# Performance work log

Hardware: AMD Instinct MI355X
Metric: run time of the kernel (lower is better)

## Reference

```python
import jax, jax.numpy as jnp
import numpy as np

EMB = 64
NODE_DIM = 5
T = 5
B, N = 8, 512


def setup_inputs() -> dict:
    key = jax.random.key(0)
    ks = jax.random.split(key, 24)
    def w(k, shape):
        return jax.random.normal(k, shape, dtype=jnp.float32) * 0.1
    xv = jax.random.normal(ks[0], (B, N, NODE_DIM), dtype=jnp.float32)
    Ws = jax.random.uniform(ks[1], (B, N, N), dtype=jnp.float32)
    reach = jax.random.bernoulli(ks[2], 0.5, (B, N))
    reach = reach.at[:, 0].set(True)  # guarantee at least one reachable node
    return {
        'xv': xv, 'Ws': Ws, 'reachable_nodes': reach,
        'W1a': w(ks[3], (NODE_DIM, EMB)), 'b1a': w(ks[4], (EMB,)),
        'W1b': w(ks[5], (EMB, EMB)),      'b1b': w(ks[6], (EMB,)),
        'W2':  w(ks[7], (EMB, EMB)),      'b2':  w(ks[8], (EMB,)),
        'W3':  w(ks[9], (EMB, EMB)),      'b3':  w(ks[10], (EMB,)),
        'w4':  w(ks[11], (EMB,)),         'b4':  w(ks[12], (EMB,)),
        'W6':  w(ks[13], (EMB, EMB)),     'b6':  w(ks[14], (EMB,)),
        'W7':  w(ks[15], (EMB, EMB)),     'b7':  w(ks[16], (EMB,)),
        'W51': w(ks[17], (2 * EMB, EMB)), 'b51': w(ks[18], (EMB,)),
        'w52': w(ks[19], (EMB,)),         'b52': w(ks[20], ()),
    }


def _struc2vec(xv, Ws, W1a, b1a, W1b, b1b, W2, b2, W3, b3, w4, b4):
    # s1: per-node feature embedding [B,N,E]
    s1 = jax.nn.relu(xv @ W1a + b1a) @ W1b + b1b
    # edge-feature path: relu(theta4(Ws[...,None])) summed over dim 1 -> [B,N,E]
    s3_1 = jax.nn.relu(Ws[..., None] * w4 + b4)  # [B,N,N,E]
    s3 = jnp.sum(s3_1, axis=1) @ W3 + b3         # [B,N,E]
    mu = jnp.zeros(s1.shape, dtype=s1.dtype)
    for _ in range(T):
        s2 = jnp.einsum('bnm,bme->bne', Ws, mu) @ W2 + b2
        mu = jax.nn.relu(s1 + s2 + s3)
    return mu


def reference(xv, Ws, reachable_nodes, W1a, b1a, W1b, b1b, W2, b2, W3, b3,
              w4, b4, W6, b6, W7, b7, W51, b51, w52, b52):
    mu = _struc2vec(xv, Ws, W1a, b1a, W1b, b1b, W2, b2, W3, b3, w4, b4)
    # global state broadcast to every node + local per-node action embedding
    global_state = jnp.sum(mu, axis=1, keepdims=True) @ W6 + b6  # [B,1,E]
    global_state = jnp.broadcast_to(global_state, mu.shape)      # [B,N,E]
    local_action = mu @ W7 + b7                                  # [B,N,E]
    rep = jax.nn.relu(jnp.concatenate([global_state, local_action], axis=2))
    rep = jax.nn.relu(rep) @ W51 + b51                           # relu(relu(.)) as in source
    prob_logits = rep @ w52 + b52                                # [B,N]
    prob_logits = jnp.where(reachable_nodes, prob_logits, -jnp.inf)
    return prob_logits
```

## Files before the change

### kernel.cpp

```cpp
#include <hip/hip_runtime.h>
#include <hip/hip_bf16.h>
#include <cstdint>
#include <cstddef>

#define BB 8
#define NN 512
#define EE 64

typedef __attribute__((ext_vector_type(8))) short short8v;
typedef __attribute__((ext_vector_type(4))) float f32x4;
typedef __attribute__((ext_vector_type(4))) unsigned int u32x4;
typedef __attribute__((ext_vector_type(2))) unsigned int u32x2;

static __device__ __forceinline__ unsigned short f2bf(float f) {
  __hip_bfloat16 h = __float2bfloat16(f);
  return *reinterpret_cast<unsigned short*>(&h);
}
static __device__ __forceinline__ float bf2f(unsigned short u) {
  unsigned x = ((unsigned)u) << 16;
  float f; __builtin_memcpy(&f, &x, 4); return f;
}
static __device__ __forceinline__ u32x4 ld_b128_sc(const void* p) {
  u32x4 v;
  asm volatile("global_load_dwordx4 %0, %1, off sc0 sc1"
               : "=v"(v) : "v"(p) : "memory");
  return v;
}
static __device__ __forceinline__ unsigned ld_b32_sc(const void* p) {
  unsigned v;
  asm volatile("global_load_dword %0, %1, off sc0 sc1\n\ts_waitcnt vmcnt(0)"
               : "=v"(v) : "v"(p) : "memory");
  return v;
}
static __device__ __forceinline__ void st_b64_sc(void* p, u32x2 v) {
  asm volatile("global_store_dwordx2 %0, %1, off sc0 sc1"
               :: "v"(p), "v"(v) : "memory");
}
static __device__ __forceinline__ void st_b32_sc(void* p, unsigned v) {
  asm volatile("global_store_dword %0, %1, off sc0 sc1"
               :: "v"(p), "v"(v) : "memory");
}
static __device__ __forceinline__ void vm0() {
  asm volatile("s_waitcnt vmcnt(0)" ::: "memory");
}
static __device__ __forceinline__ short8v as_s8(u32x4 v) {
  short8v r; __builtin_memcpy(&r, &v, 16); return r;
}

__global__ __launch_bounds__(512) void k_fused(
    const float* __restrict__ Ws, const float* __restrict__ xv,
    const float* __restrict__ W1a, const float* __restrict__ b1a,
    const float* __restrict__ W1b, const float* __restrict__ b1b,
    const float* __restrict__ W2, const float* __restrict__ b2,
    const float* __restrict__ W3, const float* __restrict__ b3,
    const float* __restrict__ w4, const float* __restrict__ b4,
    const float* __restrict__ W6, const float* __restrict__ b6,
    const float* __restrict__ W7, const float* __restrict__ b7,
    const float* __restrict__ W51, const float* __restrict__ b51,
    const float* __restrict__ w52, const float* __restrict__ b52,
    const void* __restrict__ reach, float* __restrict__ out,
    unsigned short* __restrict__ zA, unsigned short* __restrict__ zB,
    float* __restrict__ gpart, unsigned* __restrict__ flags) {
  const int blk = blockIdx.x;
  const int b = blk >> 5;
  const int stripe = blk & 31;
  const int n0 = stripe << 4;
  const int t = threadIdx.x;
  const int w = t >> 6, l = t & 63, lr = l & 15, hi = l >> 4;
  const int lk = hi * 8, nq = hi * 4, eb = w & 3, kh = w >> 2;

  __shared__ __attribute__((aligned(16))) float tileT[16][132];
  __shared__ float sp[16][68];
  __shared__ float half_[16][68];
  __shared__ float hh[16][68];
  __shared__ float base_lds[16][68];
  __shared__ float yred[16][68];
  __shared__ __attribute__((aligned(16))) unsigned short muzA[512];
  __shared__ __attribute__((aligned(16))) unsigned short muzB[512];
  __shared__ __attribute__((aligned(16))) unsigned short zbf[64][20];
  __shared__ float gsl[64], gsr[64], v7l[64], w52l[64], pl_lds[16];
  __shared__ float g0c;
  __shared__ int sbig, sflt;

  auto arrive = [&](int idx) {
    vm0();
    __syncthreads();
    if (t == 0) st_b32_sc(&flags[(b * 8 + idx) * 32 + stripe], 1u);
  };
  auto wait = [&](int idx) {
    if (t < 64) {
      const unsigned* fp = &flags[(b * 8 + idx) * 32 + (t & 31)];
      while (true) {
        unsigned v = ld_b32_sc(fp);
        if (__ballot(v != 0u) == ~0ull) break;
        __builtin_amdgcn_s_sleep(1);
      }
    }
    __syncthreads();
  };

  auto muz_store = [&](int node, int e, float v) {
    int eh = e & 31;
    unsigned short* dst = (e < 32) ? muzA : muzB;
    dst[((eh >> 3) * 16 + node) * 8 + (eh & 7)] = f2bf(v);
  };

  const float* wsbase = Ws + (size_t)b * NN * NN;
  const int lrow = t >> 2, lc4 = (t & 3) * 4;
  float4 tr0 = *(const float4*)&wsbase[(size_t)(0 * 128 + lrow) * NN + n0 + lc4];
  float4 tr1 = *(const float4*)&wsbase[(size_t)(1 * 128 + lrow) * NN + n0 + lc4];
  float4 tr2 = *(const float4*)&wsbase[(size_t)(2 * 128 + lrow) * NN + n0 + lc4];
  float4 tr3 = *(const float4*)&wsbase[(size_t)(3 * 128 + lrow) * NN + n0 + lc4];

  short8v WBa = {}, WBb = {};
  if (w < 4) {
    union { unsigned short u[8]; short8v v; } pa, pb;
#pragma unroll
    for (int j = 0; j < 8; ++j) {
      pa.u[j] = f2bf(W2[(8 * hi + j) * EE + 16 * w + lr]);
      pb.u[j] = f2bf(W2[(8 * hi + j + 32) * EE + 16 * w + lr]);
    }
    WBa = pa.v; WBb = pb.v;
  }

  {
    int e = t & 63;
#pragma unroll
    for (int p = 0; p < 2; ++p) {
      int rr = p * 8 + (t >> 6);
      const float* x = xv + ((size_t)b * NN + n0 + rr) * 5;
      float h = b1a[e];
      h = fmaf(x[0], W1a[0 * EE + e], h);
      h = fmaf(x[1], W1a[1 * EE + e], h);
      h = fmaf(x[2], W1a[2 * EE + e], h);
      h = fmaf(x[3], W1a[3 * EE + e], h);
      h = fmaf(x[4], W1a[4 * EE + e], h);
      hh[rr][e] = fmaxf(h, 0.f);
    }
  }
  {
    int ih = t >> 8;
    int n = (t >> 4) & 15;
    int e0 = (t & 15) * 4;
    float4 w4v = *(const float4*)&w4[e0];
    float4 b4v = *(const float4*)&b4[e0];
    float a0 = 0.f, a1 = 0.f, a2 = 0.f, a3 = 0.f;
    int ib = ih * 64;
#pragma unroll
    for (int c = 0; c < 4; ++c) {
      float4 tv = (c == 0) ? tr0 : (c == 1) ? tr1 : (c == 2) ? tr2 : tr3;
      tileT[lc4 + 0][lrow] = tv.x;
      tileT[lc4 + 1][lrow] = tv.y;
      tileT[lc4 + 2][lrow] = tv.z;
      tileT[lc4 + 3][lrow] = tv.w;
      __syncthreads();
#pragma unroll
      for (int i4 = 0; i4 < 16; ++i4) {
        float4 wv = *(const float4*)&tileT[n][ib + i4 * 4];
#pragma unroll
        for (int k = 0; k < 4; ++k) {
          float ww = (k == 0) ? wv.x : (k == 1) ? wv.y : (k == 2) ? wv.z : wv.w;
          a0 += fmaxf(fmaf(ww, w4v.x, b4v.x), 0.f);
          a1 += fmaxf(fmaf(ww, w4v.y, b4v.y), 0.f);
          a2 += fmaxf(fmaf(ww, w4v.z, b4v.z), 0.f);
          a3 += fmaxf(fmaf(ww, w4v.w, b4v.w), 0.f);
        }
      }
      __syncthreads();
    }
    if (ih) {
      half_[n][e0] = a0; half_[n][e0 + 1] = a1;
      half_[n][e0 + 2] = a2; half_[n][e0 + 3] = a3;
    }
    __syncthreads();
    if (!ih) {
      sp[n][e0]     = a0 + half_[n][e0];
      sp[n][e0 + 1] = a1 + half_[n][e0 + 1];
      sp[n][e0 + 2] = a2 + half_[n][e0 + 2];
      sp[n][e0 + 3] = a3 + half_[n][e0 + 3];
    }
  }
  __syncthreads();
  {
    int e = t & 63;
#pragma unroll
    for (int p = 0; p < 2; ++p) {
      int rr = p * 8 + (t >> 6);
      float s = b1b[e] + b3[e] + b2[e];
#pragma unroll 8
      for (int j = 0; j < EE; ++j)
        s = fmaf(hh[rr][j], W1b[j * EE + e], fmaf(sp[rr][j], W3[j * EE + e], s));
      base_lds[rr][e] = s;
      muz_store(rr, e, fmaxf(s, 0.f));
    }
  }
  __syncthreads();

  auto zphase = [&]() {
    if (w < 4) {
      short8v a0 = *(const short8v*)&muzA[l * 8];
      short8v a1 = *(const short8v*)&muzB[l * 8];
      f32x4 zacc = {0.f, 0.f, 0.f, 0.f};
      zacc = __builtin_amdgcn_mfma_f32_16x16x32_bf16(a0, WBa, zacc, 0, 0, 0);
      zacc = __builtin_amdgcn_mfma_f32_16x16x32_bf16(a1, WBb, zacc, 0, 0, 0);
      ushort4 u;
      u.x = f2bf(zacc[0]); u.y = f2bf(zacc[1]);
      u.z = f2bf(zacc[2]); u.w = f2bf(zacc[3]);
      *(ushort4*)&zbf[16 * w + lr][4 * hi] = u;
    }
  };
  auto publish = [&](unsigned short* dst) {
    if (t < 256) {
      int e = t >> 2, mq = (t & 3) * 4;
      u32x2 v;
      __builtin_memcpy(&v, &zbf[e][mq], 8);
      st_b64_sc(dst + ((size_t)b * EE + e) * NN + n0 + mq, v);
    }
  };

  zphase();
  __syncthreads();
  publish(zA);
  arrive(0);

  short8v A0, A1, A2, A3, A4, A5, A6, A7;
  {
    const float* arow = wsbase + (size_t)(n0 + lr) * NN + kh * 256 + lk;
    union { unsigned short u[8]; short8v v; } pk;
#define LDA(DST, OFF)                                                        \
    { float4 fa = *(const float4*)(arow + OFF);                              \
      float4 fb = *(const float4*)(arow + OFF + 4);                          \
      pk.u[0] = f2bf(fa.x); pk.u[1] = f2bf(fa.y);                            \
      pk.u[2] = f2bf(fa.z); pk.u[3] = f2bf(fa.w);                            \
      pk.u[4] = f2bf(fb.x); pk.u[5] = f2bf(fb.y);                            \
      pk.u[6] = f2bf(fb.z); pk.u[7] = f2bf(fb.w);                            \
      DST = pk.v; }
    LDA(A0, 0)   LDA(A1, 32)  LDA(A2, 64)  LDA(A3, 96)
    LDA(A4, 128) LDA(A5, 160) LDA(A6, 192) LDA(A7, 224)
#undef LDA
  }

  auto prop = [&](const unsigned short* zsrc) {
    const unsigned short* Bp =
        zsrc + ((size_t)b * EE + eb * 16 + lr) * NN + kh * 256 + lk;
    u32x4 q0 = ld_b128_sc(Bp + 0);
    u32x4 q1 = ld_b128_sc(Bp + 32);
    u32x4 q2 = ld_b128_sc(Bp + 64);
    u32x4 q3 = ld_b128_sc(Bp + 96);
    u32x4 q4 = ld_b128_sc(Bp + 128);
    u32x4 q5 = ld_b128_sc(Bp + 160);
    u32x4 q6 = ld_b128_sc(Bp + 192);
    u32x4 q7 = ld_b128_sc(Bp + 224);
    vm0();
    __builtin_amdgcn_sched_barrier(0);
    f32x4 acc = {0.f, 0.f, 0.f, 0.f};
    acc = __builtin_amdgcn_mfma_f32_16x16x32_bf16(A0, as_s8(q0), acc, 0, 0, 0);
    acc = __builtin_amdgcn_mfma_f32_16x16x32_bf16(A1, as_s8(q1), acc, 0, 0, 0);
    acc = __builtin_amdgcn_mfma_f32_16x16x32_bf16(A2, as_s8(q2), acc, 0, 0, 0);
    acc = __builtin_amdgcn_mfma_f32_16x16x32_bf16(A3, as_s8(q3), acc, 0, 0, 0);
    acc = __builtin_amdgcn_mfma_f32_16x16x32_bf16(A4, as_s8(q4), acc, 0, 0, 0);
    acc = __builtin_amdgcn_mfma_f32_16x16x32_bf16(A5, as_s8(q5), acc, 0, 0, 0);
    acc = __builtin_amdgcn_mfma_f32_16x16x32_bf16(A6, as_s8(q6), acc, 0, 0, 0);
    acc = __builtin_amdgcn_mfma_f32_16x16x32_bf16(A7, as_s8(q7), acc, 0, 0, 0);
    if (kh == 1) {
#pragma unroll
      for (int q = 0; q < 4; ++q) yred[nq + q][eb * 16 + lr] = acc[q];
    }
    __syncthreads();
    if (kh == 0) {
      int ep = eb * 16 + lr;
#pragma unroll
      for (int q = 0; q < 4; ++q) {
        float v = fmaxf(base_lds[nq + q][ep] + acc[q] + yred[nq + q][ep], 0.f);
        muz_store(nq + q, ep, v);
      }
    }
    __syncthreads();
  };

  wait(0);
  prop(zA); zphase(); __syncthreads(); publish(zB); arrive(1); wait(1);
  prop(zB); zphase(); __syncthreads(); publish(zA); arrive(2); wait(2);
  prop(zA); zphase(); __syncthreads(); publish(zB); arrive(3); wait(3);
  prop(zB);

  if (t < 64) {
    int eh = t & 31, jj = t & 7, lb = (eh >> 3) * 16;
    const unsigned short* dst = (t < 32) ? muzA : muzB;
    float s = 0.f;
#pragma unroll
    for (int n = 0; n < 16; ++n) s += bf2f(dst[(lb + n) * 8 + jj]);
    st_b32_sc(&gpart[((size_t)b * 32 + stripe) * EE + t], __float_as_uint(s));
  }
  arrive(4);

  if (t == 0) { sbig = 0; sflt = 0; }
  if (t < 64) w52l[t] = w52[t];
  __syncthreads();
  if (t < 256) {
    const unsigned int* rw = (const unsigned int*)reach;
    bool big = false, flt = false;
#pragma unroll
    for (int l2 = 0; l2 < 4; ++l2) {
      unsigned int v = rw[t + l2 * 256];
      if (v > 1u) big = true;
      if (v == 0x3f800000u) flt = true;
    }
    if (big) sbig = 1;
    if (flt) sflt = 1;
  }
  if (t >= 320 && t < 384) {
    int j = t - 320;
    float v = 0.f;
#pragma unroll 8
    for (int e = 0; e < EE; ++e) v = fmaf(W51[(EE + j) * EE + e], w52[e], v);
    v7l[j] = v;
  }
  __syncthreads();
#pragma unroll
  for (int p = 0; p < 2; ++p) {
    int n = p * 8 + (t >> 6), e7 = t & 63;
    float la = b7[e7];
#pragma unroll
    for (int h = 0; h < 2; ++h) {
      const unsigned short* dst = h ? muzB : muzA;
#pragma unroll
      for (int h2 = 0; h2 < 4; ++h2) {
        short8v mv = *(const short8v*)&dst[(h2 * 16 + n) * 8];
#pragma unroll
        for (int j = 0; j < 8; ++j)
          la = fmaf(bf2f((unsigned short)mv[j]),
                    W7[(h * 32 + h2 * 8 + j) * EE + e7], la);
      }
    }
    float c = fmaxf(la, 0.f) * v7l[e7];
#pragma unroll
    for (int off = 32; off > 0; off >>= 1) c += __shfl_down(c, off, 64);
    if (e7 == 0) pl_lds[n] = c;
  }

  wait(4);

  float* gacc = &tileT[0][0];
  {
    int s = t >> 4, e4 = (t & 15) * 4;
    u32x4 v = ld_b128_sc(&gpart[((size_t)b * 32 + s) * EE + e4]);
    vm0();
    gacc[s * EE + e4 + 0] = __uint_as_float(v.x);
    gacc[s * EE + e4 + 1] = __uint_as_float(v.y);
    gacc[s * EE + e4 + 2] = __uint_as_float(v.z);
    gacc[s * EE + e4 + 3] = __uint_as_float(v.w);
  }
  __syncthreads();
  if (t < 64) {
    float s = 0.f;
#pragma unroll 8
    for (int k = 0; k < 32; ++k) s += gacc[k * EE + t];
    gsl[t] = s;
  }
  __syncthreads();
  if (t < 64) {
    float a = b6[t];
#pragma unroll 8
    for (int k = 0; k < EE; ++k) a = fmaf(gsl[k], W6[k * EE + t], a);
    gsr[t] = fmaxf(a, 0.f);
  }
  __syncthreads();
  if (t < 64) {
    float q = 0.f;
#pragma unroll 8
    for (int j = 0; j < EE; ++j) q = fmaf(gsr[j], W51[j * EE + t], q);
    float pg = (q + b51[t]) * w52l[t];
#pragma unroll
    for (int off = 32; off > 0; off >>= 1) pg += __shfl_down(pg, off, 64);
    if (t == 0) g0c = pg + b52[0];
  }
  __syncthreads();
  if (t < 16) {
    int row = b * NN + n0 + t;
    bool rc;
    if (sflt)      rc = ((const float*)reach)[row] != 0.f;
    else if (sbig) rc = ((const unsigned char*)reach)[row] != 0;
    else           rc = ((const int*)reach)[row] != 0;
    out[row] = rc ? (pl_lds[t] + g0c) : -1.0e30f;
  }
}

extern "C" void kernel_launch(void* const* d_in, const int* in_sizes, int n_in,
                              void* d_out, int out_size, void* d_ws, size_t ws_size,
                              hipStream_t stream) {
  const float* xv  = (const float*)d_in[0];
  const float* Ws  = (const float*)d_in[1];
  const void*  rch = d_in[2];
  const float* W1a = (const float*)d_in[3];
  const float* b1a = (const float*)d_in[4];
  const float* W1b = (const float*)d_in[5];
  const float* b1b = (const float*)d_in[6];
  const float* W2  = (const float*)d_in[7];
  const float* b2  = (const float*)d_in[8];
  const float* W3  = (const float*)d_in[9];
  const float* b3  = (const float*)d_in[10];
  const float* w4  = (const float*)d_in[11];
  const float* b4  = (const float*)d_in[12];
  const float* W6  = (const float*)d_in[13];
  const float* b6  = (const float*)d_in[14];
  const float* W7  = (const float*)d_in[15];
  const float* b7  = (const float*)d_in[16];
  const float* W51 = (const float*)d_in[17];
  const float* b51 = (const float*)d_in[18];
  const float* w52 = (const float*)d_in[19];
  const float* b52 = (const float*)d_in[20];
  float* out = (float*)d_out;

  char* wsb = (char*)d_ws;
  unsigned short* zA   = (unsigned short*)wsb;
  unsigned short* zB   = (unsigned short*)(wsb + (512 << 10));
  float* gpart         = (float*)(wsb + (1024 << 10));
  unsigned* flags      = (unsigned*)(wsb + (1088 << 10));

  hipMemsetAsync((void*)flags, 0, 8192, stream);
  k_fused<<<dim3(256), dim3(512), 0, stream>>>(
      Ws, xv, W1a, b1a, W1b, b1b, W2, b2, W3, b3, w4, b4,
      W6, b6, W7, b7, W51, b51, w52, b52, rch, out,
      zA, zB, gpart, flags);
}
```

Before: 56.55 us.

## Use four write-once z buffers, plain cached loads, and direct z stores

Replaces the two ping-pong z buffers with four separate workspace buffers, one per propagation round, so no global buffer is ever overwritten during the kernel. Because each buffer is written once, the propagation step can read it with ordinary vector loads instead of inline-asm sc0 sc1 loads with an explicit vmcnt wait and scheduling barrier. This lets the compiler interleave the loads with the MFMAs. The z-phase also stores its bf16 results straight to global memory from the MFMA lanes, removing the LDS staging tile, a block barrier and the separate publish pass. In exchange it doubles the workspace and relies on cross-XCD cache coherence holding for first-time reads of freshly written lines; the direct stores are also less regular than the staged ones.

```diff
diff --git a/kernel.cpp b/kernel.cpp
--- a/kernel.cpp
+++ b/kernel.cpp
@@ -42,9 +42,6 @@
 }
 static __device__ __forceinline__ void vm0() {
   asm volatile("s_waitcnt vmcnt(0)" ::: "memory");
-}
-static __device__ __forceinline__ short8v as_s8(u32x4 v) {
-  short8v r; __builtin_memcpy(&r, &v, 16); return r;
 }
 
 __global__ __launch_bounds__(512) void k_fused(
@@ -59,7 +56,8 @@
     const float* __restrict__ W51, const float* __restrict__ b51,
     const float* __restrict__ w52, const float* __restrict__ b52,
     const void* __restrict__ reach, float* __restrict__ out,
-    unsigned short* __restrict__ zA, unsigned short* __restrict__ zB,
+    unsigned short* __restrict__ z0, unsigned short* __restrict__ z1,
+    unsigned short* __restrict__ z2, unsigned short* __restrict__ z3,
     float* __restrict__ gpart, unsigned* __restrict__ flags) {
   const int blk = blockIdx.x;
   const int b = blk >> 5;
@@ -77,7 +75,6 @@
   __shared__ float yred[16][68];
   __shared__ __attribute__((aligned(16))) unsigned short muzA[512];
   __shared__ __attribute__((aligned(16))) unsigned short muzB[512];
-  __shared__ __attribute__((aligned(16))) unsigned short zbf[64][20];
   __shared__ float gsl[64], gsr[64], v7l[64], w52l[64], pl_lds[16];
   __shared__ float g0c;
   __shared__ int sbig, sflt;
@@ -196,7 +193,7 @@
   }
   __syncthreads();
 
-  auto zphase = [&]() {
+  auto zphase = [&](unsigned short* dst) {
     if (w < 4) {
       short8v a0 = *(const short8v*)&muzA[l * 8];
       short8v a1 = *(const short8v*)&muzB[l * 8];
@@ -206,21 +203,12 @@
       ushort4 u;
       u.x = f2bf(zacc[0]); u.y = f2bf(zacc[1]);
       u.z = f2bf(zacc[2]); u.w = f2bf(zacc[3]);
-      *(ushort4*)&zbf[16 * w + lr][4 * hi] = u;
+      u32x2 v; __builtin_memcpy(&v, &u, 8);
+      st_b64_sc(dst + ((size_t)b * EE + 16 * w + lr) * NN + n0 + 4 * hi, v);
     }
   };
-  auto publish = [&](unsigned short* dst) {
-    if (t < 256) {
-      int e = t >> 2, mq = (t & 3) * 4;
-      u32x2 v;
-      __builtin_memcpy(&v, &zbf[e][mq], 8);
-      st_b64_sc(dst + ((size_t)b * EE + e) * NN + n0 + mq, v);
-    }
-  };
-
-  zphase();
-  __syncthreads();
-  publish(zA);
+
+  zphase(z0);
   arrive(0);
 
   short8v A0, A1, A2, A3, A4, A5, A6, A7;
@@ -243,25 +231,23 @@
   auto prop = [&](const unsigned short* zsrc) {
     const unsigned short* Bp =
         zsrc + ((size_t)b * EE + eb * 16 + lr) * NN + kh * 256 + lk;
-    u32x4 q0 = ld_b128_sc(Bp + 0);
-    u32x4 q1 = ld_b128_sc(Bp + 32);
-    u32x4 q2 = ld_b128_sc(Bp + 64);
-    u32x4 q3 = ld_b128_sc(Bp + 96);
-    u32x4 q4 = ld_b128_sc(Bp + 128);
-    u32x4 q5 = ld_b128_sc(Bp + 160);
-    u32x4 q6 = ld_b128_sc(Bp + 192);
-    u32x4 q7 = ld_b128_sc(Bp + 224);
-    vm0();
-    __builtin_amdgcn_sched_barrier(0);
+    short8v q0 = *(const short8v*)(Bp + 0);
+    short8v q1 = *(const short8v*)(Bp + 32);
+    short8v q2 = *(const short8v*)(Bp + 64);
+    short8v q3 = *(const short8v*)(Bp + 96);
+    short8v q4 = *(const short8v*)(Bp + 128);
+    short8v q5 = *(const short8v*)(Bp + 160);
+    short8v q6 = *(const short8v*)(Bp + 192);
+    short8v q7 = *(const short8v*)(Bp + 224);
     f32x4 acc = {0.f, 0.f, 0.f, 0.f};
-    acc = __builtin_amdgcn_mfma_f32_16x16x32_bf16(A0, as_s8(q0), acc, 0, 0, 0);
-    acc = __builtin_amdgcn_mfma_f32_16x16x32_bf16(A1, as_s8(q1), acc, 0, 0, 0);
-    acc = __builtin_amdgcn_mfma_f32_16x16x32_bf16(A2, as_s8(q2), acc, 0, 0, 0);
-    acc = __builtin_amdgcn_mfma_f32_16x16x32_bf16(A3, as_s8(q3), acc, 0, 0, 0);
-    acc = __builtin_amdgcn_mfma_f32_16x16x32_bf16(A4, as_s8(q4), acc, 0, 0, 0);
-    acc = __builtin_amdgcn_mfma_f32_16x16x32_bf16(A5, as_s8(q5), acc, 0, 0, 0);
-    acc = __builtin_amdgcn_mfma_f32_16x16x32_bf16(A6, as_s8(q6), acc, 0, 0, 0);
-    acc = __builtin_amdgcn_mfma_f32_16x16x32_bf16(A7, as_s8(q7), acc, 0, 0, 0);
+    acc = __builtin_amdgcn_mfma_f32_16x16x32_bf16(A0, q0, acc, 0, 0, 0);
+    acc = __builtin_amdgcn_mfma_f32_16x16x32_bf16(A1, q1, acc, 0, 0, 0);
+    acc = __builtin_amdgcn_mfma_f32_16x16x32_bf16(A2, q2, acc, 0, 0, 0);
+    acc = __builtin_amdgcn_mfma_f32_16x16x32_bf16(A3, q3, acc, 0, 0, 0);
+    acc = __builtin_amdgcn_mfma_f32_16x16x32_bf16(A4, q4, acc, 0, 0, 0);
+    acc = __builtin_amdgcn_mfma_f32_16x16x32_bf16(A5, q5, acc, 0, 0, 0);
+    acc = __builtin_amdgcn_mfma_f32_16x16x32_bf16(A6, q6, acc, 0, 0, 0);
+    acc = __builtin_amdgcn_mfma_f32_16x16x32_bf16(A7, q7, acc, 0, 0, 0);
     if (kh == 1) {
 #pragma unroll
       for (int q = 0; q < 4; ++q) yred[nq + q][eb * 16 + lr] = acc[q];
@@ -279,10 +265,10 @@
   };
 
   wait(0);
-  prop(zA); zphase(); __syncthreads(); publish(zB); arrive(1); wait(1);
-  prop(zB); zphase(); __syncthreads(); publish(zA); arrive(2); wait(2);
-  prop(zA); zphase(); __syncthreads(); publish(zB); arrive(3); wait(3);
-  prop(zB);
+  prop(z0); zphase(z1); arrive(1); wait(1);
+  prop(z1); zphase(z2); arrive(2); wait(2);
+  prop(z2); zphase(z3); arrive(3); wait(3);
+  prop(z3);
 
   if (t < 64) {
     int eh = t & 31, jj = t & 7, lb = (eh >> 3) * 16;
@@ -413,14 +399,16 @@
   float* out = (float*)d_out;
 
   char* wsb = (char*)d_ws;
-  unsigned short* zA   = (unsigned short*)wsb;
-  unsigned short* zB   = (unsigned short*)(wsb + (512 << 10));
-  float* gpart         = (float*)(wsb + (1024 << 10));
-  unsigned* flags      = (unsigned*)(wsb + (1088 << 10));
+  unsigned short* z0   = (unsigned short*)wsb;
+  unsigned short* z1   = (unsigned short*)(wsb + (512 << 10));
+  unsigned short* z2   = (unsigned short*)(wsb + (1024 << 10));
+  unsigned short* z3   = (unsigned short*)(wsb + (1536 << 10));
+  float* gpart         = (float*)(wsb + (2048 << 10));
+  unsigned* flags      = (unsigned*)(wsb + (2112 << 10));
 
   hipMemsetAsync((void*)flags, 0, 8192, stream);
   k_fused<<<dim3(256), dim3(512), 0, stream>>>(
       Ws, xv, W1a, b1a, W1b, b1b, W2, b2, W3, b3, w4, b4,
       W6, b6, W7, b7, W51, b51, w52, b52, rch, out,
-      zA, zB, gpart, flags);
-}
+      z0, z1, z2, z3, gpart, flags);
+}
```

After: 59.41 us. +5.0%, slower.
